# Optimization experiments

Hardware: AMD Instinct MI355X
Metric: run time of the kernel (lower is better)

Reference implementation:

```python
import jax, jax.numpy as jnp
import numpy as np

V = 100000          # vocab size
D = 256             # hidden dim
B, N = 32, 128      # batch, max_len
K = 100             # noise_ratio
NORM_TERM = 11.512925  # log(V), norm_term='auto'
BACKOFF_PROB = 1e-10


def setup_inputs() -> dict:
    key = jax.random.key(0)
    ks = jax.random.split(key, 6)
    target = jax.random.randint(ks[0], (B, N), 0, V)
    noise_samples = jax.random.randint(ks[1], (B, N, K), 0, V)
    hidden = jax.random.normal(ks[2], (B, N, D), dtype=jnp.float32) * 0.1
    weight = jax.random.normal(ks[3], (V, D), dtype=jnp.float32) * 0.05
    bias = jax.random.normal(ks[4], (V,), dtype=jnp.float32) * 0.01
    u = jax.random.uniform(ks[5], (V,), dtype=jnp.float32) + BACKOFF_PROB
    noise_probs = u / jnp.sum(u)  # normalized noise distribution
    return {"target": target, "noise_samples": noise_samples, "hidden": hidden,
            "weight": weight, "bias": bias, "noise_probs": noise_probs}


def reference(target, noise_samples, hidden, weight, bias, noise_probs):
    # score_noise = log P_noise(noise_samples)   (B,N,K) -- irregular gather on (V,)
    score_noise = jnp.log(noise_probs)[noise_samples]
    # get_score (IndexLinear): gathered output-embedding dot products
    w_t = weight[target]                                   # (B,N,D)
    score_model = jnp.einsum('bnd,bnd->bn', hidden, w_t) + bias[target] - NORM_TERM
    w_n = weight[noise_samples]                            # (B,N,K,D) big gather
    score_noise_in_model = (jnp.einsum('bnd,bnkd->bnk', hidden, w_n)
                            + bias[noise_samples] - NORM_TERM)
    # NCE binary classification loss (score_target_in_noise passed as zeros)
    log_k = jnp.log(jnp.float32(K))
    logit_true = score_model - log_k                        # (B,N) label=1
    logit_noise = score_noise_in_model - score_noise - log_k  # (B,N,K) label=0
    # BCE-with-logits: -log sigmoid(x) = softplus(-x); -log(1-sigmoid(x)) = softplus(x)
    loss = jax.nn.softplus(-logit_true) + jnp.sum(jax.nn.softplus(logit_noise), axis=-1)
    # reduction='elementwise_mean'
    return jnp.mean(loss)
```

## Files before the change

### kernel.cpp

```cpp
#include <hip/hip_runtime.h>
#include <math.h>

#define V 100000
#define D 256
#define B 32
#define N 128
#define K 100
#define NPOS (B * N)
#define NPAIR (NPOS * (K + 1))
#define BIN_ROWS 32
#define NBIN (V / BIN_ROWS)
#define NSHARD 8
#define CAP_S 56
#define MAXTOT (NSHARD * CAP_S)
#define SLAB_W (D + 8)
#define NORM_TERM 11.512925f
#define LOG_K 4.605170186f

typedef float f32x4 __attribute__((ext_vector_type(4)));
typedef unsigned short u16;

__device__ __forceinline__ float softplus(float x) {
    return fmaxf(x, 0.f) + __logf(1.f + __expf(-fabsf(x)));
}
__device__ __forceinline__ unsigned f32_to_bf16_bits(float x) {
    unsigned u = __float_as_uint(x);
    u += 0x7FFFu + ((u >> 16) & 1u);
    return u >> 16;
}

__global__ __launch_bounds__(256) void scatter_kernel(
    const int* __restrict__ target, const int* __restrict__ noise,
    int* __restrict__ cursor, unsigned* __restrict__ buf)
{
    const int p = blockIdx.x * 256 + threadIdx.x;
    if (p >= NPAIR) return;
    int row, pos; unsigned flag;
    if (p < NPOS * K) { pos = p / K; row = noise[p]; flag = 0u; }
    else              { pos = p - NPOS * K; row = target[pos]; flag = 1u; }
    const int bin   = row >> 5;
    const int shard = blockIdx.x & (NSHARD - 1);
    const int cell  = bin * NSHARD + shard;
    const int slot  = atomicAdd(&cursor[cell], 1);
    if (slot < CAP_S)
        buf[(size_t)cell * CAP_S + slot] =
            ((unsigned)(row & (BIN_ROWS - 1)) << 13) | ((unsigned)pos << 1) | flag;
}

__global__ __launch_bounds__(256, 8) void compute_kernel(
    const float* __restrict__ hidden, const float* __restrict__ weight,
    const float* __restrict__ bias, const float* __restrict__ noise_probs,
    const int* __restrict__ cursor, const unsigned* __restrict__ buf,
    float* __restrict__ out)
{
    __shared__ u16      slab[BIN_ROWS * SLAB_W];
    __shared__ float    sbias[BIN_ROWS];
    __shared__ float    slogp[BIN_ROWS];
    __shared__ unsigned plist[MAXTOT];
    __shared__ int      scnt[NSHARD];
    __shared__ int      pref[NSHARD + 1];
    __shared__ float    wsum[4];

    const int bin = blockIdx.x;
    const int tid = threadIdx.x;

    if (tid < NSHARD)
        scnt[tid] = min(cursor[bin * NSHARD + tid], CAP_S);
    __syncthreads();
    if (tid == 0) {
        int s = 0;
        #pragma unroll
        for (int i = 0; i < NSHARD; ++i) { pref[i] = s; s += scnt[i]; }
        pref[NSHARD] = s;
    }
    __syncthreads();
    const int total = pref[NSHARD];
    if (total == 0) return;

    const int wave = tid >> 6;
    const int lane = tid & 63;
    const int q    = lane >> 4;
    const int ql   = lane & 15;
    const int row0 = bin * BIN_ROWS;

    for (int r = wave; r < BIN_ROWS; r += 4) {
        const f32x4 w4 = __builtin_nontemporal_load(
            (const f32x4*)(weight + (size_t)(row0 + r) * D + lane * 4));
        uint2 b;
        b.x = f32_to_bf16_bits(w4.x) | (f32_to_bf16_bits(w4.y) << 16);
        b.y = f32_to_bf16_bits(w4.z) | (f32_to_bf16_bits(w4.w) << 16);
        *(uint2*)(slab + r * SLAB_W + lane * 4) = b;
    }
    if (tid < BIN_ROWS) {
        sbias[tid] = bias[row0 + tid];
        slogp[tid] = __logf(noise_probs[row0 + tid]);
    }
    for (int i = tid; i < total; i += 256) {
        int s = 0;
        #pragma unroll
        for (int j = 1; j < NSHARD; ++j) s += (i >= pref[j]);
        plist[i] = buf[((size_t)(bin * NSHARD + s)) * CAP_S + (i - pref[s])];
    }
    __syncthreads();

    float loss = 0.f;
    for (int base = wave * 4; base < total; base += 16) {
        const int p = base + q;
        const bool valid = (p < total);
        const unsigned rec = valid ? plist[p] : 0u;
        const int rloc = (int)((rec >> 13) & (BIN_ROWS - 1));
        const int pos  = (int)((rec >> 1) & (NPOS - 1));

        const float* __restrict__ hp = hidden + (size_t)pos * D + ql * 4;
        const u16*   __restrict__ wp = slab + rloc * SLAB_W + ql * 4;
        float acc = 0.f;
        #pragma unroll
        for (int i = 0; i < 4; ++i) {
            const f32x4 h4 = *(const f32x4*)(hp + i * 64);
            const uint2 wb = *(const uint2*)(wp + i * 64);
            acc = fmaf(__uint_as_float(wb.x << 16),          h4.x, acc);
            acc = fmaf(__uint_as_float(wb.x & 0xffff0000u),  h4.y, acc);
            acc = fmaf(__uint_as_float(wb.y << 16),          h4.z, acc);
            acc = fmaf(__uint_as_float(wb.y & 0xffff0000u),  h4.w, acc);
        }
        #pragma unroll
        for (int off = 1; off < 16; off <<= 1)
            acc += __shfl_xor(acc, off, 64);

        const float score = acc + sbias[rloc] - NORM_TERM;
        const float contrib = (rec & 1u)
            ? softplus(LOG_K - score)
            : softplus(score - slogp[rloc] - LOG_K);
        if (valid && ql == 0) loss += contrib;
    }

    loss += __shfl_xor(loss, 16, 64);
    loss += __shfl_xor(loss, 32, 64);
    if (lane == 0) wsum[wave] = loss;
    __syncthreads();
    if (tid == 0)
        atomicAdd(out, (wsum[0] + wsum[1] + wsum[2] + wsum[3])
                       * (1.0f / (float)NPOS));
}

extern "C" void kernel_launch(void* const* d_in, const int* in_sizes, int n_in,
                              void* d_out, int out_size, void* d_ws, size_t ws_size,
                              hipStream_t stream) {
    const int*   target      = (const int*)d_in[0];
    const int*   noise       = (const int*)d_in[1];
    const float* hidden      = (const float*)d_in[2];
    const float* weight      = (const float*)d_in[3];
    const float* bias        = (const float*)d_in[4];
    const float* noise_probs = (const float*)d_in[5];
    float* out = (float*)d_out;

    int*      cursor = (int*)d_ws;
    unsigned* buf    = (unsigned*)((char*)d_ws + (size_t)NBIN * NSHARD * 4);

    hipMemsetAsync(cursor, 0, (size_t)NBIN * NSHARD * 4, stream);
    hipMemsetAsync(out, 0, sizeof(float), stream);

    scatter_kernel<<<(NPAIR + 255) / 256, 256, 0, stream>>>(
        target, noise, cursor, buf);
    compute_kernel<<<NBIN, 256, 0, stream>>>(
        hidden, weight, bias, noise_probs, cursor, buf, out);
}
```

Before: 226.6 us.

## Software-pipeline hidden/slab loads in compute loop and use DPP quarter reductions

The per-pair dot-product loop now keeps two iterations of hidden rows and bf16 weight slab data in registers, prefetching the next records while the current one is computed, to hide gather latency on hidden. The 16-lane shuffle reduction becomes a DPP-based quarter-row sum, and the FMA chain is split into four independent accumulators. The scatter uses 16 shards with capacity 32 instead of 8 with 56, and the occupancy hint drops from 8 to 6 blocks to make room for the extra prefetch registers, at the cost of fewer resident waves.

```diff
diff --git a/kernel.cpp b/kernel.cpp
--- a/kernel.cpp
+++ b/kernel.cpp
@@ -10,8 +10,8 @@
 #define NPAIR (NPOS * (K + 1))
 #define BIN_ROWS 32
 #define NBIN (V / BIN_ROWS)
-#define NSHARD 8
-#define CAP_S 56
+#define NSHARD 16
+#define CAP_S 32
 #define MAXTOT (NSHARD * CAP_S)
 #define SLAB_W (D + 8)
 #define NORM_TERM 11.512925f
@@ -27,6 +27,20 @@
     unsigned u = __float_as_uint(x);
     u += 0x7FFFu + ((u >> 16) & 1u);
     return u >> 16;
+}
+
+template <int CTRL>
+__device__ __forceinline__ float dpp_add(float x) {
+    int y = __builtin_amdgcn_update_dpp(__float_as_int(x), __float_as_int(x),
+                                        CTRL, 0xF, 0xF, false);
+    return x + __int_as_float(y);
+}
+__device__ __forceinline__ float quarter_sum(float x) {
+    x = dpp_add<0xB1>(x);
+    x = dpp_add<0x4E>(x);
+    x = dpp_add<0x141>(x);
+    x = dpp_add<0x140>(x);
+    return x;
 }
 
 __global__ __launch_bounds__(256) void scatter_kernel(
@@ -47,7 +61,7 @@
             ((unsigned)(row & (BIN_ROWS - 1)) << 13) | ((unsigned)pos << 1) | flag;
 }
 
-__global__ __launch_bounds__(256, 8) void compute_kernel(
+__global__ __launch_bounds__(256, 6) void compute_kernel(
     const float* __restrict__ hidden, const float* __restrict__ weight,
     const float* __restrict__ bias, const float* __restrict__ noise_probs,
     const int* __restrict__ cursor, const unsigned* __restrict__ buf,
@@ -103,35 +117,73 @@
     }
     __syncthreads();
 
+    const int p0 = wave * 4 + q;
+
+    unsigned rec_c  = (p0      < total) ? plist[p0]      : 0u;
+    unsigned rec_nx = (p0 + 16 < total) ? plist[p0 + 16] : 0u;
+
+    f32x4 hc[4], hn[4];
+    uint2 wc[4], wn[4];
+
+    {
+        const float* hp = hidden + (size_t)((rec_c >> 1) & (NPOS - 1)) * D + ql * 4;
+        const u16*   wp = slab + ((rec_c >> 13) & (BIN_ROWS - 1)) * SLAB_W + ql * 4;
+        #pragma unroll
+        for (int i = 0; i < 4; ++i) {
+            hc[i] = *(const f32x4*)(hp + i * 64);
+            wc[i] = *(const uint2*)(wp + i * 64);
+        }
+        const float* hp2 = hidden + (size_t)((rec_nx >> 1) & (NPOS - 1)) * D + ql * 4;
+        const u16*   wp2 = slab + ((rec_nx >> 13) & (BIN_ROWS - 1)) * SLAB_W + ql * 4;
+        #pragma unroll
+        for (int i = 0; i < 4; ++i) {
+            hn[i] = *(const f32x4*)(hp2 + i * 64);
+            wn[i] = *(const uint2*)(wp2 + i * 64);
+        }
+    }
+
     float loss = 0.f;
     for (int base = wave * 4; base < total; base += 16) {
         const int p = base + q;
-        const bool valid = (p < total);
-        const unsigned rec = valid ? plist[p] : 0u;
-        const int rloc = (int)((rec >> 13) & (BIN_ROWS - 1));
-        const int pos  = (int)((rec >> 1) & (NPOS - 1));
-
-        const float* __restrict__ hp = hidden + (size_t)pos * D + ql * 4;
-        const u16*   __restrict__ wp = slab + rloc * SLAB_W + ql * 4;
-        float acc = 0.f;
+        const unsigned rec_2 = (p + 32 < total) ? plist[p + 32] : 0u;
+
+        float s0 = 0.f, s1 = 0.f, s2 = 0.f, s3 = 0.f;
+        s0 = fmaf(__uint_as_float(wc[0].x << 16),         hc[0].x, s0);
+        s0 = fmaf(__uint_as_float(wc[0].x & 0xffff0000u), hc[0].y, s0);
+        s0 = fmaf(__uint_as_float(wc[0].y << 16),         hc[0].z, s0);
+        s0 = fmaf(__uint_as_float(wc[0].y & 0xffff0000u), hc[0].w, s0);
+        s1 = fmaf(__uint_as_float(wc[1].x << 16),         hc[1].x, s1);
+        s1 = fmaf(__uint_as_float(wc[1].x & 0xffff0000u), hc[1].y, s1);
+        s1 = fmaf(__uint_as_float(wc[1].y << 16),         hc[1].z, s1);
+        s1 = fmaf(__uint_as_float(wc[1].y & 0xffff0000u), hc[1].w, s1);
+        s2 = fmaf(__uint_as_float(wc[2].x << 16),         hc[2].x, s2);
+        s2 = fmaf(__uint_as_float(wc[2].x & 0xffff0000u), hc[2].y, s2);
+        s2 = fmaf(__uint_as_float(wc[2].y << 16),         hc[2].z, s2);
+        s2 = fmaf(__uint_as_float(wc[2].y & 0xffff0000u), hc[2].w, s2);
+        s3 = fmaf(__uint_as_float(wc[3].x << 16),         hc[3].x, s3);
+        s3 = fmaf(__uint_as_float(wc[3].x & 0xffff0000u), hc[3].y, s3);
+        s3 = fmaf(__uint_as_float(wc[3].y << 16),         hc[3].z, s3);
+        s3 = fmaf(__uint_as_float(wc[3].y & 0xffff0000u), hc[3].w, s3);
+
+        const float r = quarter_sum((s0 + s1) + (s2 + s3));
+
+        const int rloc = (int)((rec_c >> 13) & (BIN_ROWS - 1));
+        const float score = r + sbias[rloc] - NORM_TERM;
+        const float x = (rec_c & 1u) ? (LOG_K - score)
+                                     : (score - slogp[rloc] - LOG_K);
+        if ((p < total) && ql == 0) loss += softplus(x);
+
+        rec_c  = rec_nx;
+        rec_nx = rec_2;
+        #pragma unroll
+        for (int i = 0; i < 4; ++i) { hc[i] = hn[i]; wc[i] = wn[i]; }
+        const float* hp = hidden + (size_t)((rec_nx >> 1) & (NPOS - 1)) * D + ql * 4;
+        const u16*   wp = slab + ((rec_nx >> 13) & (BIN_ROWS - 1)) * SLAB_W + ql * 4;
         #pragma unroll
         for (int i = 0; i < 4; ++i) {
-            const f32x4 h4 = *(const f32x4*)(hp + i * 64);
-            const uint2 wb = *(const uint2*)(wp + i * 64);
-            acc = fmaf(__uint_as_float(wb.x << 16),          h4.x, acc);
-            acc = fmaf(__uint_as_float(wb.x & 0xffff0000u),  h4.y, acc);
-            acc = fmaf(__uint_as_float(wb.y << 16),          h4.z, acc);
-            acc = fmaf(__uint_as_float(wb.y & 0xffff0000u),  h4.w, acc);
+            hn[i] = *(const f32x4*)(hp + i * 64);
+            wn[i] = *(const uint2*)(wp + i * 64);
         }
-        #pragma unroll
-        for (int off = 1; off < 16; off <<= 1)
-            acc += __shfl_xor(acc, off, 64);
-
-        const float score = acc + sbias[rloc] - NORM_TERM;
-        const float contrib = (rec & 1u)
-            ? softplus(LOG_K - score)
-            : softplus(score - slogp[rloc] - LOG_K);
-        if (valid && ql == 0) loss += contrib;
     }
 
     loss += __shfl_xor(loss, 16, 64);
```

After: 223.7 us. No clear change (-1.3%).

## Convert hidden and weights to fp16 and use packed dot2 with DPP reductions

Applied to the files above, without the earlier changes.

The scatter kernel now also converts the hidden activations to a packed fp16 table, and the weight slab in shared memory is stored as fp16 instead of bf16. The inner dot product uses the fdot2 intrinsic on 128-bit loads, and the 16-lane reduction uses DPP adds instead of shuffles. Sharding changes from 8x56 to 16x32 slots per bin, which halves the gathered hidden traffic and cuts instruction count. The trade-off is lower precision and a smaller per-shard capacity, which makes it more likely that overflowing entries are silently dropped.

```diff
diff --git a/kernel.cpp b/kernel.cpp
--- a/kernel.cpp
+++ b/kernel.cpp
@@ -10,50 +10,90 @@
 #define NPAIR (NPOS * (K + 1))
 #define BIN_ROWS 32
 #define NBIN (V / BIN_ROWS)
-#define NSHARD 8
-#define CAP_S 56
+#define NSHARD 16
+#define CAP_S 32
 #define MAXTOT (NSHARD * CAP_S)
-#define SLAB_W (D + 8)
+#define ROW_W32 136
+#define HVEC (NPOS * D / 4)
 #define NORM_TERM 11.512925f
 #define LOG_K 4.605170186f
 
-typedef float f32x4 __attribute__((ext_vector_type(4)));
-typedef unsigned short u16;
+typedef float    f32x4 __attribute__((ext_vector_type(4)));
+typedef unsigned u32x2 __attribute__((ext_vector_type(2)));
+typedef unsigned u32x4 __attribute__((ext_vector_type(4)));
+typedef __fp16   f16x2 __attribute__((ext_vector_type(2)));
 
 __device__ __forceinline__ float softplus(float x) {
     return fmaxf(x, 0.f) + __logf(1.f + __expf(-fabsf(x)));
 }
-__device__ __forceinline__ unsigned f32_to_bf16_bits(float x) {
-    unsigned u = __float_as_uint(x);
-    u += 0x7FFFu + ((u >> 16) & 1u);
-    return u >> 16;
-}
-
-__global__ __launch_bounds__(256) void scatter_kernel(
+
+__device__ __forceinline__ unsigned pack_f16(float a, float b) {
+#if __has_builtin(__builtin_amdgcn_cvt_pkrtz)
+    f16x2 h = __builtin_amdgcn_cvt_pkrtz(a, b);
+#else
+    f16x2 h; h.x = (__fp16)a; h.y = (__fp16)b;
+#endif
+    union { f16x2 h; unsigned u; } c; c.h = h;
+    return c.u;
+}
+
+#if __has_builtin(__builtin_amdgcn_fdot2)
+#define DOT2(a, b, c) __builtin_amdgcn_fdot2((a), (b), (c), false)
+#else
+__device__ __forceinline__ float DOT2(f16x2 a, f16x2 b, float c) {
+    return fmaf((float)a.x, (float)b.x, fmaf((float)a.y, (float)b.y, c));
+}
+#endif
+
+union V4H { u32x4 u; f16x2 h[4]; };
+
+template <int CTRL>
+__device__ __forceinline__ float dpp_add(float x) {
+    int y = __builtin_amdgcn_update_dpp(__float_as_int(x), __float_as_int(x),
+                                        CTRL, 0xF, 0xF, false);
+    return x + __int_as_float(y);
+}
+__device__ __forceinline__ float quarter_sum(float x) {
+    x = dpp_add<0xB1>(x);
+    x = dpp_add<0x4E>(x);
+    x = dpp_add<0x141>(x);
+    x = dpp_add<0x140>(x);
+    return x;
+}
+
+__global__ __launch_bounds__(256) void scatter_hconv_kernel(
     const int* __restrict__ target, const int* __restrict__ noise,
-    int* __restrict__ cursor, unsigned* __restrict__ buf)
+    const float* __restrict__ hidden,
+    int* __restrict__ cursor, unsigned* __restrict__ buf,
+    unsigned* __restrict__ htab32)
 {
     const int p = blockIdx.x * 256 + threadIdx.x;
-    if (p >= NPAIR) return;
+
     int row, pos; unsigned flag;
     if (p < NPOS * K) { pos = p / K; row = noise[p]; flag = 0u; }
     else              { pos = p - NPOS * K; row = target[pos]; flag = 1u; }
-    const int bin   = row >> 5;
-    const int shard = blockIdx.x & (NSHARD - 1);
-    const int cell  = bin * NSHARD + shard;
-    const int slot  = atomicAdd(&cursor[cell], 1);
+    const int cell = (row >> 5) * NSHARD + (blockIdx.x & (NSHARD - 1));
+    const int slot = atomicAdd(&cursor[cell], 1);
     if (slot < CAP_S)
         buf[(size_t)cell * CAP_S + slot] =
             ((unsigned)(row & (BIN_ROWS - 1)) << 13) | ((unsigned)pos << 1) | flag;
+
+    if (p < HVEC) {
+        const f32x4 h4 = *((const f32x4*)hidden + p);
+        u32x2 o;
+        o.x = pack_f16(h4.x, h4.y);
+        o.y = pack_f16(h4.z, h4.w);
+        *(u32x2*)(htab32 + (size_t)p * 2) = o;
+    }
 }
 
 __global__ __launch_bounds__(256, 8) void compute_kernel(
-    const float* __restrict__ hidden, const float* __restrict__ weight,
+    const unsigned* __restrict__ htab32, const float* __restrict__ weight,
     const float* __restrict__ bias, const float* __restrict__ noise_probs,
     const int* __restrict__ cursor, const unsigned* __restrict__ buf,
     float* __restrict__ out)
 {
-    __shared__ u16      slab[BIN_ROWS * SLAB_W];
+    __shared__ unsigned slab32[BIN_ROWS * ROW_W32];
     __shared__ float    sbias[BIN_ROWS];
     __shared__ float    slogp[BIN_ROWS];
     __shared__ unsigned plist[MAXTOT];
@@ -86,10 +126,10 @@
     for (int r = wave; r < BIN_ROWS; r += 4) {
         const f32x4 w4 = __builtin_nontemporal_load(
             (const f32x4*)(weight + (size_t)(row0 + r) * D + lane * 4));
-        uint2 b;
-        b.x = f32_to_bf16_bits(w4.x) | (f32_to_bf16_bits(w4.y) << 16);
-        b.y = f32_to_bf16_bits(w4.z) | (f32_to_bf16_bits(w4.w) << 16);
-        *(uint2*)(slab + r * SLAB_W + lane * 4) = b;
+        u32x2 o;
+        o.x = pack_f16(w4.x, w4.y);
+        o.y = pack_f16(w4.z, w4.w);
+        *(u32x2*)(slab32 + r * ROW_W32 + lane * 2) = o;
     }
     if (tid < BIN_ROWS) {
         sbias[tid] = bias[row0 + tid];
@@ -111,27 +151,30 @@
         const int rloc = (int)((rec >> 13) & (BIN_ROWS - 1));
         const int pos  = (int)((rec >> 1) & (NPOS - 1));
 
-        const float* __restrict__ hp = hidden + (size_t)pos * D + ql * 4;
-        const u16*   __restrict__ wp = slab + rloc * SLAB_W + ql * 4;
-        float acc = 0.f;
-        #pragma unroll
-        for (int i = 0; i < 4; ++i) {
-            const f32x4 h4 = *(const f32x4*)(hp + i * 64);
-            const uint2 wb = *(const uint2*)(wp + i * 64);
-            acc = fmaf(__uint_as_float(wb.x << 16),          h4.x, acc);
-            acc = fmaf(__uint_as_float(wb.x & 0xffff0000u),  h4.y, acc);
-            acc = fmaf(__uint_as_float(wb.y << 16),          h4.z, acc);
-            acc = fmaf(__uint_as_float(wb.y & 0xffff0000u),  h4.w, acc);
-        }
-        #pragma unroll
-        for (int off = 1; off < 16; off <<= 1)
-            acc += __shfl_xor(acc, off, 64);
-
-        const float score = acc + sbias[rloc] - NORM_TERM;
-        const float contrib = (rec & 1u)
-            ? softplus(LOG_K - score)
-            : softplus(score - slogp[rloc] - LOG_K);
-        if (valid && ql == 0) loss += contrib;
+        const u32x4* hp = (const u32x4*)(htab32 + (size_t)pos * 128) + ql;
+        V4H H0, H1, W0, W1;
+        H0.u = hp[0];
+        H1.u = hp[16];
+        const unsigned* wr = slab32 + rloc * ROW_W32;
+        W0.u = *(const u32x4*)(wr + ql * 4);
+        W1.u = *(const u32x4*)(wr + 64 + ql * 4);
+
+        float a0 = 0.f, a1 = 0.f, a2 = 0.f, a3 = 0.f;
+        a0 = DOT2(H0.h[0], W0.h[0], a0);
+        a1 = DOT2(H0.h[1], W0.h[1], a1);
+        a2 = DOT2(H0.h[2], W0.h[2], a2);
+        a3 = DOT2(H0.h[3], W0.h[3], a3);
+        a0 = DOT2(H1.h[0], W1.h[0], a0);
+        a1 = DOT2(H1.h[1], W1.h[1], a1);
+        a2 = DOT2(H1.h[2], W1.h[2], a2);
+        a3 = DOT2(H1.h[3], W1.h[3], a3);
+
+        const float r = quarter_sum((a0 + a1) + (a2 + a3));
+
+        const float score = r + sbias[rloc] - NORM_TERM;
+        const float x = (rec & 1u) ? (LOG_K - score)
+                                   : (score - slogp[rloc] - LOG_K);
+        if (valid && ql == 0) loss += softplus(x);
     }
 
     loss += __shfl_xor(loss, 16, 64);
@@ -154,14 +197,17 @@
     const float* noise_probs = (const float*)d_in[5];
     float* out = (float*)d_out;
 
+    const size_t cursor_bytes = (size_t)NBIN * NSHARD * 4;
+    const size_t buf_bytes    = (size_t)NBIN * NSHARD * CAP_S * 4;
     int*      cursor = (int*)d_ws;
-    unsigned* buf    = (unsigned*)((char*)d_ws + (size_t)NBIN * NSHARD * 4);
-
-    hipMemsetAsync(cursor, 0, (size_t)NBIN * NSHARD * 4, stream);
-    hipMemsetAsync(out, 0, sizeof(float), stream);
-
-    scatter_kernel<<<(NPAIR + 255) / 256, 256, 0, stream>>>(
-        target, noise, cursor, buf);
+    unsigned* buf    = (unsigned*)((char*)d_ws + cursor_bytes);
+    unsigned* htab32 = (unsigned*)((char*)d_ws + cursor_bytes + buf_bytes);
+
+    (void)hipMemsetAsync(cursor, 0, cursor_bytes, stream);
+    (void)hipMemsetAsync(out, 0, sizeof(float), stream);
+
+    scatter_hconv_kernel<<<NPAIR / 256, 256, 0, stream>>>(
+        target, noise, hidden, cursor, buf, htab32);
     compute_kernel<<<NBIN, 256, 0, stream>>>(
-        hidden, weight, bias, noise_probs, cursor, buf, out);
-}
+        htab32, weight, bias, noise_probs, cursor, buf, out);
+}
```

New measurement: 220.7 us. 1.03x faster.
